# Kernel optimization log

Hardware: AMD Instinct MI355X
Metric: run time of the kernel (lower is better)

Reference implementation:

```python
import jax, jax.numpy as jnp
import numpy as np
from jax import lax

NUM_STATES = 16
NUM_CHAINS = 2
NUM_NODES = 2000
NUM_ITERS = 1000


def setup_inputs() -> dict:
    key = jax.random.key(0)
    k0, k1, k2, k3 = jax.random.split(key, 4)
    return {
        "unnormalized_state_init": jax.random.normal(k0, (NUM_STATES,), dtype=jnp.float32),
        "unnormalized_chain_weights": jax.random.normal(k1, (NUM_STATES, NUM_CHAINS), dtype=jnp.float32),
        "unnormalized_emission_matrix": jax.random.normal(k2, (NUM_STATES, NUM_NODES), dtype=jnp.float32),
        "unnormalized_transition_matrix": jax.random.normal(k3, (NUM_STATES, NUM_STATES), dtype=jnp.float32),
    }


def reference(unnormalized_state_init, unnormalized_chain_weights,
              unnormalized_emission_matrix, unnormalized_transition_matrix):
    # Normalize parameters in log domain (matches torch log_softmax dims)
    log_state_init = jax.nn.log_softmax(unnormalized_state_init, axis=0)            # (S,)
    log_chain_weights = jax.nn.log_softmax(unnormalized_chain_weights, axis=1)      # (S,C)
    log_emission_matrix = jax.nn.log_softmax(unnormalized_emission_matrix, axis=1)  # (S,N)
    log_transition_matrix = jax.nn.log_softmax(unnormalized_transition_matrix, axis=1)  # (S,S)

    # Sequential HMM forward recursion in log domain:
    # h_t[j] = logsumexp_i( h_{t-1}[i] + log_T[i, j] )
    def step(h, _):
        h_next = jax.nn.logsumexp(h[:, None] + log_transition_matrix, axis=0)
        return h_next, h_next

    _, hs = lax.scan(step, log_state_init, None, length=NUM_ITERS - 1)
    log_hidden_state_probs = jnp.concatenate([log_state_init[None, :], hs], axis=0)  # (T,S)

    # P(node | state, chain, iter) joint in log domain: (T,S,C,N)
    # (original repeats emission across the 2 chains; here broadcast over C)
    log_observed_state_probs_ = (
        log_emission_matrix[None, :, None, :]
        + log_chain_weights[None, :, :, None]
        + log_hidden_state_probs[:, :, None, None]
    )
    # Marginalize states then chains (logsumexp over axes 1 then 1 == axes (1,2))
    log_observed_state_probs = jax.nn.logsumexp(log_observed_state_probs_, axis=(1, 2))  # (T,N)
    return log_observed_state_probs
```

## Files before the change

### kernel.cpp

```cpp
#include <hip/hip_runtime.h>
#include <math.h>

#define NN 2000

__global__ __launch_bounds__(256) void ssm_fused(
    const float* __restrict__ init,
    const float* __restrict__ emis,
    const float* __restrict__ trans,
    float* __restrict__ out)
{
  __shared__ float Tp[16][16];
  __shared__ float Bb[2][16][16];
  __shared__ float Rb[2][16][16];
  __shared__ float Z[16];
  __shared__ float wrow[4][16];
  __shared__ float p0v[16];

  const int tid  = threadIdx.x;
  const int i    = tid >> 4, j = tid & 15;
  const int lane = tid & 63, wv = tid >> 6;

  Rb[0][i][j] = trans[tid];

  if (tid < 16) {
    float m = -1e30f, s2 = 0.f;
    #pragma unroll
    for (int k = 0; k < 16; ++k) m = fmaxf(m, init[k]);
    #pragma unroll
    for (int k = 0; k < 16; ++k) s2 += __expf(init[k] - m);
    p0v[tid] = __expf(init[tid] - m) / s2;
  }

  float ssum[4] = {0.f, 0.f, 0.f, 0.f};
  for (int g = lane; g < 500; g += 64) {
    #pragma unroll
    for (int si = 0; si < 4; ++si) {
      const int s = wv * 4 + si;
      float4 v = *(const float4*)(emis + s * NN + g * 4);
      ssum[si] += __expf(v.x) + __expf(v.y) + __expf(v.z) + __expf(v.w);
    }
  }
  #pragma unroll
  for (int si = 0; si < 4; ++si) {
    float v = ssum[si];
    #pragma unroll
    for (int off = 32; off > 0; off >>= 1) v += __shfl_down(v, off);
    if (lane == 0) Z[wv * 4 + si] = v;
  }
  __syncthreads();

  {
    float m = -1e30f;
    #pragma unroll
    for (int k = 0; k < 16; ++k) m = fmaxf(m, Rb[0][i][k]);
    float sm = 0.f;
    #pragma unroll
    for (int k = 0; k < 16; ++k) sm += __expf(Rb[0][i][k] - m);
    const float tp = __expf(Rb[0][i][j] - m) / sm;
    __syncthreads();
    Tp[i][j] = tp;
    Bb[0][i][j] = tp;
  }
  __syncthreads();

  int bs = 0;
  #pragma unroll
  for (int q = 0; q < 2; ++q) {
    float acc = 0.f;
    #pragma unroll
    for (int k = 0; k < 16; ++k) acc += Bb[bs][i][k] * Bb[bs][k][j];
    Bb[bs ^ 1][i][j] = acc;
    __syncthreads();
    bs ^= 1;
  }

  int e = blockIdx.y;
  int rs = 0;
  bool rvalid = false;
  while (e) {
    const bool mul = (e & 1);
    float accR = 0.f, accB = 0.f;
    if (mul) {
      if (rvalid) {
        #pragma unroll
        for (int k = 0; k < 16; ++k) accR += Rb[rs][i][k] * Bb[bs][k][j];
      } else {
        accR = Bb[bs][i][j];
      }
    }
    #pragma unroll
    for (int k = 0; k < 16; ++k) accB += Bb[bs][i][k] * Bb[bs][k][j];
    if (mul) Rb[rs ^ 1][i][j] = accR;
    Bb[bs ^ 1][i][j] = accB;
    __syncthreads();
    if (mul) { rs ^= 1; rvalid = true; }
    bs ^= 1;
    e >>= 1;
  }

  if (tid < 16) {
    if (rvalid) {
      float acc = 0.f;
      #pragma unroll
      for (int k = 0; k < 16; ++k) acc += p0v[k] * Rb[rs][k][tid];
      wrow[0][tid] = acc;
    } else {
      wrow[0][tid] = p0v[tid];
    }
  }
  __syncthreads();
  for (int tt = 1; tt < 4; ++tt) {
    if (tid < 16) {
      float acc = 0.f;
      #pragma unroll
      for (int k = 0; k < 16; ++k) acc += wrow[tt - 1][k] * Tp[k][tid];
      wrow[tt][tid] = acc;
    }
    __syncthreads();
  }
  if (tid < 64) wrow[tid >> 4][tid & 15] /= Z[tid & 15];
  __syncthreads();

  const int g = blockIdx.x * 256 + tid;
  if (g < 500) {
    float4 ex[16];
    #pragma unroll
    for (int s = 0; s < 16; ++s) {
      float4 v = *(const float4*)(emis + s * NN + g * 4);
      ex[s].x = __expf(v.x); ex[s].y = __expf(v.y);
      ex[s].z = __expf(v.z); ex[s].w = __expf(v.w);
    }
    const int tbase = blockIdx.y * 4;
    #pragma unroll
    for (int tt = 0; tt < 4; ++tt) {
      float4 acc = make_float4(0.f, 0.f, 0.f, 0.f);
      #pragma unroll
      for (int s = 0; s < 16; ++s) {
        const float p = wrow[tt][s];
        acc.x += p * ex[s].x; acc.y += p * ex[s].y;
        acc.z += p * ex[s].z; acc.w += p * ex[s].w;
      }
      float4 o;
      o.x = __logf(acc.x); o.y = __logf(acc.y);
      o.z = __logf(acc.z); o.w = __logf(acc.w);
      *(float4*)(out + (tbase + tt) * NN + g * 4) = o;
    }
  }
}

extern "C" void kernel_launch(void* const* d_in, const int* in_sizes, int n_in,
                              void* d_out, int out_size, void* d_ws, size_t ws_size,
                              hipStream_t stream) {
  const float* init  = (const float*)d_in[0];
  const float* emis  = (const float*)d_in[2];
  const float* trans = (const float*)d_in[3];
  float* out = (float*)d_out;

  hipLaunchKernelGGL(ssm_fused, dim3(2, 250), dim3(256), 0, stream,
                     init, emis, trans, out);
}
```

Measured before the change: 73.61 us.

## Split into single-block prep kernel computing all state vectors by doubling, then output kernel

Replaces the per-block matrix-power computation (each of 500 blocks redundantly computing T^(4y) by repeated squaring plus the emission normalizer) with one prep kernel. That kernel builds all 1000 hidden-state probability rows via a doubling scheme in shared memory and writes them, pre-scaled by 1/Z, to workspace. The output kernel then only loads its 4 rows and does the emission mixture and log. This removes redundant per-block work and the serial sync chain, but adds a second launch and a serial single-block prep stage of about 10 doubling rounds.

```diff
diff --git a/kernel.cpp b/kernel.cpp
--- a/kernel.cpp
+++ b/kernel.cpp
@@ -2,25 +2,25 @@
 #include <math.h>
 
 #define NN 2000
+#define NT 1000
 
-__global__ __launch_bounds__(256) void ssm_fused(
+__global__ __launch_bounds__(256) void ssm_prep(
     const float* __restrict__ init,
     const float* __restrict__ emis,
     const float* __restrict__ trans,
-    float* __restrict__ out)
+    float* __restrict__ wd)
 {
-  __shared__ float Tp[16][16];
-  __shared__ float Bb[2][16][16];
-  __shared__ float Rb[2][16][16];
+  __shared__ float W[NT][17];
+  __shared__ float P[2][16][17];
   __shared__ float Z[16];
-  __shared__ float wrow[4][16];
+  __shared__ float iZv[16];
   __shared__ float p0v[16];
 
   const int tid  = threadIdx.x;
   const int i    = tid >> 4, j = tid & 15;
   const int lane = tid & 63, wv = tid >> 6;
 
-  Rb[0][i][j] = trans[tid];
+  P[1][i][j] = trans[tid];
 
   if (tid < 16) {
     float m = -1e30f, s2 = 0.f;
@@ -52,73 +52,51 @@
   {
     float m = -1e30f;
     #pragma unroll
-    for (int k = 0; k < 16; ++k) m = fmaxf(m, Rb[0][i][k]);
+    for (int k = 0; k < 16; ++k) m = fmaxf(m, P[1][i][k]);
     float sm = 0.f;
     #pragma unroll
-    for (int k = 0; k < 16; ++k) sm += __expf(Rb[0][i][k] - m);
-    const float tp = __expf(Rb[0][i][j] - m) / sm;
-    __syncthreads();
-    Tp[i][j] = tp;
-    Bb[0][i][j] = tp;
+    for (int k = 0; k < 16; ++k) sm += __expf(P[1][i][k] - m);
+    P[0][i][j] = __expf(P[1][i][j] - m) / sm;
   }
+  if (tid < 16) { W[0][tid] = p0v[tid]; iZv[tid] = 1.0f / Z[tid]; }
   __syncthreads();
 
-  int bs = 0;
-  #pragma unroll
-  for (int q = 0; q < 2; ++q) {
-    float acc = 0.f;
-    #pragma unroll
-    for (int k = 0; k < 16; ++k) acc += Bb[bs][i][k] * Bb[bs][k][j];
-    Bb[bs ^ 1][i][j] = acc;
+  int r = 1, ps = 0;
+  while (r < NT) {
+    const int nn = (r < NT - r) ? r : (NT - r);
+    for (int e = tid; e < nn * 16; e += 256) {
+      const int t = e >> 4, s = e & 15;
+      float acc = 0.f;
+      #pragma unroll
+      for (int k = 0; k < 16; ++k) acc += W[t][k] * P[ps][k][s];
+      W[r + t][s] = acc;
+    }
+    {
+      float acc2 = 0.f;
+      #pragma unroll
+      for (int k = 0; k < 16; ++k) acc2 += P[ps][i][k] * P[ps][k][j];
+      P[ps ^ 1][i][j] = acc2;
+    }
     __syncthreads();
-    bs ^= 1;
+    ps ^= 1;
+    r <<= 1;
   }
 
-  int e = blockIdx.y;
-  int rs = 0;
-  bool rvalid = false;
-  while (e) {
-    const bool mul = (e & 1);
-    float accR = 0.f, accB = 0.f;
-    if (mul) {
-      if (rvalid) {
-        #pragma unroll
-        for (int k = 0; k < 16; ++k) accR += Rb[rs][i][k] * Bb[bs][k][j];
-      } else {
-        accR = Bb[bs][i][j];
-      }
-    }
-    #pragma unroll
-    for (int k = 0; k < 16; ++k) accB += Bb[bs][i][k] * Bb[bs][k][j];
-    if (mul) Rb[rs ^ 1][i][j] = accR;
-    Bb[bs ^ 1][i][j] = accB;
-    __syncthreads();
-    if (mul) { rs ^= 1; rvalid = true; }
-    bs ^= 1;
-    e >>= 1;
+  for (int e = tid; e < NT * 16; e += 256) {
+    wd[e] = W[e >> 4][e & 15] * iZv[e & 15];
   }
+}
 
-  if (tid < 16) {
-    if (rvalid) {
-      float acc = 0.f;
-      #pragma unroll
-      for (int k = 0; k < 16; ++k) acc += p0v[k] * Rb[rs][k][tid];
-      wrow[0][tid] = acc;
-    } else {
-      wrow[0][tid] = p0v[tid];
-    }
-  }
-  __syncthreads();
-  for (int tt = 1; tt < 4; ++tt) {
-    if (tid < 16) {
-      float acc = 0.f;
-      #pragma unroll
-      for (int k = 0; k < 16; ++k) acc += wrow[tt - 1][k] * Tp[k][tid];
-      wrow[tt][tid] = acc;
-    }
-    __syncthreads();
-  }
-  if (tid < 64) wrow[tid >> 4][tid & 15] /= Z[tid & 15];
+__global__ __launch_bounds__(256) void ssm_out(
+    const float* __restrict__ emis,
+    const float* __restrict__ wd,
+    float* __restrict__ out)
+{
+  __shared__ float w[4][16];
+  const int tid = threadIdx.x;
+  const int tbase = blockIdx.y * 4;
+
+  if (tid < 64) w[tid >> 4][tid & 15] = wd[tbase * 16 + tid];
   __syncthreads();
 
   const int g = blockIdx.x * 256 + tid;
@@ -130,13 +108,13 @@
       ex[s].x = __expf(v.x); ex[s].y = __expf(v.y);
       ex[s].z = __expf(v.z); ex[s].w = __expf(v.w);
     }
-    const int tbase = blockIdx.y * 4;
     #pragma unroll
     for (int tt = 0; tt < 4; ++tt) {
+      const float* wr = w[tt];
       float4 acc = make_float4(0.f, 0.f, 0.f, 0.f);
       #pragma unroll
       for (int s = 0; s < 16; ++s) {
-        const float p = wrow[tt][s];
+        const float p = wr[s];
         acc.x += p * ex[s].x; acc.y += p * ex[s].y;
         acc.z += p * ex[s].z; acc.w += p * ex[s].w;
       }
@@ -155,7 +133,10 @@
   const float* emis  = (const float*)d_in[2];
   const float* trans = (const float*)d_in[3];
   float* out = (float*)d_out;
+  float* wd  = (float*)d_ws;
 
-  hipLaunchKernelGGL(ssm_fused, dim3(2, 250), dim3(256), 0, stream,
-                     init, emis, trans, out);
+  hipLaunchKernelGGL(ssm_prep, dim3(1), dim3(256), 0, stream,
+                     init, emis, trans, wd);
+  hipLaunchKernelGGL(ssm_out, dim3(2, 250), dim3(256), 0, stream,
+                     emis, wd, out);
 }
```

Measured after the change: 82.26 us. 1.12x slower.
